# Performance work log

Hardware: AMD Instinct MI355X
Metric: run time of the kernel (lower is better)

## Reference

```python
import jax, jax.numpy as jnp
import numpy as np

B, T, E, H, L, V = 2, 1024, 1024, 16, 4, 32000
HS = E // H
EPS = 1e-5


def layernorm(x, g, b):
    m = jnp.mean(x, axis=-1, keepdims=True)
    v = jnp.mean((x - m) ** 2, axis=-1, keepdims=True)
    return (x - m) * jax.lax.rsqrt(v + EPS) * g + b


def setup_inputs() -> dict:
    key = jax.random.key(0)
    ks = jax.random.split(key, 20)
    s = 0.02
    inp = {
        "ids": jax.random.randint(ks[0], (B, T), 0, V, dtype=jnp.int32),
        "emb": jax.random.normal(ks[1], (V, E), jnp.float32) * s,
        "pos": jax.random.normal(ks[2], (T, E), jnp.float32) * s,
        "wq": jax.random.normal(ks[3], (L, E, E), jnp.float32) * s,
        "bq": jnp.zeros((L, E), jnp.float32),
        "wk": jax.random.normal(ks[4], (L, E, E), jnp.float32) * s,
        "bk": jnp.zeros((L, E), jnp.float32),
        "wv": jax.random.normal(ks[5], (L, E, E), jnp.float32) * s,
        "bv": jnp.zeros((L, E), jnp.float32),
        "w1": jax.random.normal(ks[6], (L, E, 4 * E), jnp.float32) * s,
        "b1": jnp.zeros((L, 4 * E), jnp.float32),
        "w2": jax.random.normal(ks[7], (L, 4 * E, E), jnp.float32) * s,
        "b2": jnp.zeros((L, E), jnp.float32),
        "ln1_g": jnp.ones((L, E), jnp.float32),
        "ln1_b": jnp.zeros((L, E), jnp.float32),
        "ln2_g": jnp.ones((L, E), jnp.float32),
        "ln2_b": jnp.zeros((L, E), jnp.float32),
        "proj_w": jax.random.normal(ks[8], (E, V), jnp.float32) * s,
        "proj_b": jnp.zeros((V,), jnp.float32),
    }
    return inp


def reference(ids, emb, pos, wq, bq, wk, bk, wv, bv, w1, b1, w2, b2,
              ln1_g, ln1_b, ln2_g, ln2_b, proj_w, proj_b):
    x = emb[ids] + pos[:ids.shape[-1]]  # [B,T,E]
    scale = 1.0 / (E ** 0.5)  # NOTE: original divides by embed_size**0.5
    causal = jnp.tril(jnp.ones((T, T), dtype=bool))
    for l in range(L):
        h = layernorm(x, ln1_g[l], ln1_b[l])
        q = (h @ wq[l] + bq[l]).reshape(B, T, H, HS).transpose(0, 2, 1, 3)
        k = (h @ wk[l] + bk[l]).reshape(B, T, H, HS).transpose(0, 2, 1, 3)
        v = (h @ wv[l] + bv[l]).reshape(B, T, H, HS).transpose(0, 2, 1, 3)
        scores = jnp.einsum('bhqd,bhkd->bhqk', q, k) * scale
        scores = jnp.where(causal, scores, -jnp.inf)
        attn = jax.nn.softmax(scores, axis=-1)
        o = jnp.einsum('bhqk,bhkd->bhqd', attn, v)
        o = o.transpose(0, 2, 1, 3).reshape(B, T, E)
        x = x + o
        h2 = layernorm(x, ln2_g[l], ln2_b[l])
        ff = jax.nn.gelu(h2 @ w1[l] + b1[l], approximate=False) @ w2[l] + b2[l]
        x = x + ff  # Dropout(0.2) in eval mode = identity
    logits = x @ proj_w + proj_b  # [B,T,V]
    return logits
```

## Files before the change

### kernel.cpp

```cpp
#include <hip/hip_runtime.h>
#include <hip/hip_bf16.h>
#include <cstdint>

#define B_    2
#define T_    1024
#define E_    1024
#define H_    16
#define HS_   64
#define L_    4
#define V_    32000
#define FF_   4096
#define BT_   2048
#define EPS_  1e-5f
#define SCALE_ 0.03125f

typedef __bf16 bf16;
typedef bf16  bf16x4 __attribute__((ext_vector_type(4)));
typedef bf16  bf16x8 __attribute__((ext_vector_type(8)));
typedef float f32x4  __attribute__((ext_vector_type(4)));

#define GL2LDS(gp, lp) __builtin_amdgcn_global_load_lds( \
    (const __attribute__((address_space(1))) void*)(gp), \
    (__attribute__((address_space(3))) void*)(lp), 16, 0, 0)

__global__ __launch_bounds__(256) void embed_kernel(
    const int* __restrict__ ids, const float* __restrict__ emb,
    const float* __restrict__ pos, float* __restrict__ x)
{
  int bt = blockIdx.x;
  int t  = bt & (T_ - 1);
  int id = ids[bt];
  f32x4 e = *(const f32x4*)(emb + (size_t)id * E_ + threadIdx.x * 4);
  f32x4 p = *(const f32x4*)(pos + (size_t)t  * E_ + threadIdx.x * 4);
  *(f32x4*)(x + (size_t)bt * E_ + threadIdx.x * 4) = e + p;
}

__device__ __forceinline__ float wred_sum(float v) {
#pragma unroll
  for (int o = 32; o; o >>= 1) v += __shfl_xor(v, o, 64);
  return v;
}

__global__ __launch_bounds__(256) void ln_kernel(
    const float* __restrict__ x, const float* __restrict__ g,
    const float* __restrict__ b, bf16* __restrict__ h)
{
  int row = blockIdx.x, tid = threadIdx.x;
  f32x4 v = *(const f32x4*)(x + (size_t)row * E_ + tid * 4);
  float s  = v[0] + v[1] + v[2] + v[3];
  float sq = v[0]*v[0] + v[1]*v[1] + v[2]*v[2] + v[3]*v[3];
  s  = wred_sum(s);
  sq = wred_sum(sq);
  __shared__ float rs[4], rq[4];
  int w = tid >> 6, lane = tid & 63;
  if (lane == 0) { rs[w] = s; rq[w] = sq; }
  __syncthreads();
  float S = rs[0] + rs[1] + rs[2] + rs[3];
  float Q = rq[0] + rq[1] + rq[2] + rq[3];
  float mean = S * (1.0f / E_);
  float var  = Q * (1.0f / E_) - mean * mean;
  float rstd = rsqrtf(fmaxf(var, 0.0f) + EPS_);
  f32x4 gv = *(const f32x4*)(g + tid * 4);
  f32x4 bv = *(const f32x4*)(b + tid * 4);
  f32x4 o = (v - mean) * rstd * gv + bv;
  bf16x4 ob = { (bf16)o[0], (bf16)o[1], (bf16)o[2], (bf16)o[3] };
  *(bf16x4*)(h + (size_t)row * E_ + tid * 4) = ob;
}

__global__ __launch_bounds__(256) void convw_kernel(
    const float* __restrict__ W0, const float* __restrict__ W1, const float* __restrict__ W2,
    bf16* __restrict__ O0, bf16* __restrict__ O1, bf16* __restrict__ O2,
    int K, int ldW)
{
  int z = blockIdx.z;
  const float* W = (z == 0) ? W0 : (z == 1) ? W1 : W2;
  bf16*        O = (z == 0) ? O0 : (z == 1) ? O1 : O2;
  __shared__ float tl[32][33];
  int n0 = blockIdx.x * 32, k0 = blockIdx.y * 32;
  int c = threadIdx.x & 31, r = threadIdx.x >> 5;
#pragma unroll
  for (int p = 0; p < 4; ++p)
    tl[r + p * 8][c] = W[(size_t)(k0 + r + p * 8) * ldW + n0 + c];
  __syncthreads();
#pragma unroll
  for (int p = 0; p < 4; ++p)
    O[(size_t)(n0 + r + p * 8) * K + k0 + c] = (bf16)tl[c][r + p * 8];
}

template <int ACT, int MODE>
__global__ __launch_bounds__(256) void gemm_bf16(
    const bf16* __restrict__ A,
    const bf16* __restrict__ B0, const bf16* __restrict__ B1, const bf16* __restrict__ B2,
    const float* __restrict__ bi0, const float* __restrict__ bi1, const float* __restrict__ bi2,
    bf16* __restrict__ Cb0, bf16* __restrict__ Cb1, bf16* __restrict__ Cb2,
    float* __restrict__ Cf, const float* __restrict__ R,
    int K, int ldc, int LDK)
{
  int z = blockIdx.z;
  const bf16*  Bm = (MODE == 3) ? B0 : (z == 0) ? B0 : (z == 1) ? B1 : B2;
  const float* bi = (z == 0) ? bi0 : (z == 1) ? bi1 : bi2;
  bf16*        Cb = (z == 0) ? Cb0 : (z == 1) ? Cb1 : Cb2;
  int koff = (MODE == 3) ? z * K : 0;

  int nb  = (int)(gridDim.x * gridDim.y);
  int lin = blockIdx.x + gridDim.x * blockIdx.y;
  int per = nb >> 3;
  int b   = (lin & 7) * per + (lin >> 3);
  int mi  = b & 15;
  int ni  = b >> 4;

  __shared__ __align__(16) char lds[2][16384];

  int tid = threadIdx.x;
  int lane = tid & 63, wid = tid >> 6;
  int wm = (wid >> 1) * 64, wn = (wid & 1) * 64;
  int fr = lane & 15, fb = lane >> 4;

  const bf16* Asrc = A  + (size_t)(mi * 128) * LDK + koff;
  const bf16* Bsrc = Bm + (size_t)(ni * 128) * LDK + koff;

  int NT = K >> 5;

#define STAGE(buf, kk)                                                          \
  {                                                                             \
    _Pragma("unroll")                                                           \
    for (int is = 0; is < 2; ++is) {                                            \
      int rl = is * 64 + (tid >> 2);                                            \
      int key = (rl >> 1) & 3;                                                  \
      int ck  = ((tid & 3) ^ key) * 8;                                          \
      GL2LDS(Asrc + (size_t)rl * LDK + (kk) + ck,                               \
             lds[buf] + is * 4096 + tid * 16);                                  \
      GL2LDS(Bsrc + (size_t)rl * LDK + (kk) + ck,                               \
             lds[buf] + 8192 + is * 4096 + tid * 16);                           \
    }                                                                           \
  }

  f32x4 acc[4][4];
#pragma unroll
  for (int i = 0; i < 4; ++i)
#pragma unroll
    for (int j = 0; j < 4; ++j) acc[i][j] = (f32x4){0.f, 0.f, 0.f, 0.f};

  STAGE(0, 0);
  int cur = 0;

  for (int t = 0; t < NT; ++t) {
    __syncthreads();
    if (t + 1 < NT) STAGE(cur ^ 1, (t + 1) << 5);

    const char* Ab = lds[cur];
    const char* Bb = lds[cur] + 8192;
    bf16x8 af[4], bfr[4];
#pragma unroll
    for (int i = 0; i < 4; ++i) {
      int rl = wm + i * 16 + fr;
      af[i] = *(const bf16x8*)(Ab + rl * 64 + ((fb ^ ((rl >> 1) & 3)) * 16));
    }
#pragma unroll
    for (int j = 0; j < 4; ++j) {
      int rl = wn + j * 16 + fr;
      bfr[j] = *(const bf16x8*)(Bb + rl * 64 + ((fb ^ ((rl >> 1) & 3)) * 16));
    }
#pragma unroll
    for (int i = 0; i < 4; ++i)
#pragma unroll
      for (int j = 0; j < 4; ++j)
        acc[i][j] = __builtin_amdgcn_mfma_f32_16x16x32_bf16(af[i], bfr[j], acc[i][j], 0, 0, 0);
    cur ^= 1;
  }
#undef STAGE

#pragma unroll
  for (int i = 0; i < 4; ++i) {
#pragma unroll
    for (int j = 0; j < 4; ++j) {
      int gc = ni * 128 + wn + j * 16 + fr;
      float bv = (MODE == 3) ? 0.f : bi[gc];
#pragma unroll
      for (int r = 0; r < 4; ++r) {
        int gr = mi * 128 + wm + i * 16 + fb * 4 + r;
        float vv = acc[i][j][r] + bv;
        if (ACT == 1) vv = 0.5f * vv * (1.0f + erff(vv * 0.70710678118654752f));
        if (MODE == 2) {
          float nv = vv + R[(size_t)gr * ldc + gc];
          Cf[(size_t)gr * ldc + gc] = nv;
          Cb[(size_t)gr * ldc + gc] = (bf16)nv;
        } else if (MODE == 1) {
          Cb[(size_t)gr * ldc + gc] = (bf16)vv;
        } else if (MODE == 3) {
          Cf[(size_t)(z * BT_ + gr) * ldc + gc] = vv;
        }
      }
    }
  }
}

__global__ __launch_bounds__(256) void combine_kernel(
    const float* __restrict__ p, const float* __restrict__ bi,
    float* __restrict__ x, bf16* __restrict__ xb)
{
  int row = blockIdx.x, tid = threadIdx.x;
  size_t off = (size_t)row * E_ + tid * 4;
  f32x4 a = *(const f32x4*)(p + off);
  f32x4 c = *(const f32x4*)(p + (size_t)BT_ * E_ + off);
  f32x4 bv = *(const f32x4*)(bi + tid * 4);
  f32x4 xv = *(const f32x4*)(x + off);
  f32x4 nv = xv + a + c + bv;
  *(f32x4*)(x + off) = nv;
  bf16x4 ob = { (bf16)nv[0], (bf16)nv[1], (bf16)nv[2], (bf16)nv[3] };
  *(bf16x4*)(xb + off) = ob;
}

__global__ __launch_bounds__(512, 2) void gemm256_kernel(
    const bf16* __restrict__ A, const bf16* __restrict__ Bm,
    const float* __restrict__ bi, float* __restrict__ C, int K, int N)
{
  int nwg = (int)gridDim.x;
  int per = nwg >> 3;
  int bid = (int)blockIdx.x;
  int tl  = (bid & 7) * per + (bid >> 3);
  int mi  = tl & 7, ni = tl >> 3;

  __shared__ __align__(16) char lds[2][65536];

  int tid = threadIdx.x;
  int lane = tid & 63, wid = tid >> 6;
  int wr = wid >> 2, wc = wid & 3;
  int fr = lane & 15, fb = lane >> 4;

  const bf16* Asrc = A  + (size_t)(mi * 256) * K;
  const bf16* Bsrc = Bm + (size_t)(ni * 256) * K;

  int NT = K >> 6;

#define STAGE256(buf, kk)                                                  \
  { _Pragma("unroll")                                                      \
    for (int h = 0; h < 2; ++h) {                                          \
      _Pragma("unroll")                                                    \
      for (int is = 0; is < 2; ++is) {                                     \
        int ri  = is * 64 + (tid >> 3);                                    \
        int ck  = (tid & 7) ^ (ri & 7);                                    \
        int row = h * 128 + ri;                                            \
        GL2LDS(Asrc + (size_t)row * K + (kk) + ck * 8,                     \
               lds[buf] + h * 16384 + is * 8192 + tid * 16);               \
        GL2LDS(Bsrc + (size_t)row * K + (kk) + ck * 8,                     \
               lds[buf] + 32768 + h * 16384 + is * 8192 + tid * 16);       \
      }                                                                    \
    } }

  f32x4 acc[8][4];
#pragma unroll
  for (int i = 0; i < 8; ++i)
#pragma unroll
    for (int j = 0; j < 4; ++j) acc[i][j] = (f32x4){0.f, 0.f, 0.f, 0.f};

  STAGE256(0, 0);

  for (int t = 0; t < NT; ++t) {
    int buf = t & 1;
    if (t + 1 < NT) {
      STAGE256(buf ^ 1, (t + 1) << 6);
      asm volatile("s_waitcnt vmcnt(8)" ::: "memory");
    } else {
      asm volatile("s_waitcnt vmcnt(0)" ::: "memory");
    }
    __builtin_amdgcn_s_barrier();
    asm volatile("" ::: "memory");

    const char* Ab = lds[buf];
    const char* Bb = lds[buf] + 32768;

    bf16x8 bfr[4][2];
#pragma unroll
    for (int n2 = 0; n2 < 4; ++n2) {
      int row = wc * 64 + n2 * 16 + fr;
#pragma unroll
      for (int ks = 0; ks < 2; ++ks)
        bfr[n2][ks] = *(const bf16x8*)(Bb + (row >> 7) * 16384 + (row & 127) * 128
                                          + ((((ks * 4 + fb) ^ (fr & 7))) << 4));
    }
#pragma unroll
    for (int q = 0; q < 4; ++q) {
      bf16x8 af[2][2];
#pragma unroll
      for (int m2 = 0; m2 < 2; ++m2) {
        int ri = (q * 2 + m2) * 16 + fr;
#pragma unroll
        for (int ks = 0; ks < 2; ++ks)
          af[m2][ks] = *(const bf16x8*)(Ab + wr * 16384 + ri * 128
                                           + ((((ks * 4 + fb) ^ (fr & 7))) << 4));
      }
      __builtin_amdgcn_s_setprio(1);
#pragma unroll
      for (int m2 = 0; m2 < 2; ++m2)
#pragma unroll
        for (int n2 = 0; n2 < 4; ++n2)
#pragma unroll
          for (int ks = 0; ks < 2; ++ks)
            acc[q * 2 + m2][n2] = __builtin_amdgcn_mfma_f32_16x16x32_bf16(
                af[m2][ks], bfr[n2][ks], acc[q * 2 + m2][n2], 0, 0, 0);
      __builtin_amdgcn_s_setprio(0);
    }
    asm volatile("" ::: "memory");
    __builtin_amdgcn_s_barrier();
  }
#undef STAGE256

#pragma unroll
  for (int i = 0; i < 8; ++i) {
#pragma unroll
    for (int j = 0; j < 4; ++j) {
      int gc = ni * 256 + wc * 64 + j * 16 + fr;
      float bv = bi[gc];
#pragma unroll
      for (int r = 0; r < 4; ++r) {
        int gr = mi * 256 + wr * 128 + i * 16 + fb * 4 + r;
        C[(size_t)gr * N + gc] = acc[i][j][r] + bv;
      }
    }
  }
}

__global__ __launch_bounds__(256) void attn_kernel(
    const bf16* __restrict__ q, const bf16* __restrict__ k,
    const bf16* __restrict__ v, float* __restrict__ x)
{
  __shared__ __align__(16) char Ks[8192];
  __shared__ __align__(16) char Vs[8192];
  __shared__ __align__(16) char Ps[8192];

  int tid = threadIdx.x, lane = tid & 63, w = tid >> 6;
  int qt = blockIdx.x, bh = blockIdx.y;
  int b = bh >> 4, h = bh & 15;
  size_t hoff = (size_t)b * T_ * E_ + h * HS_;
  int fr = lane & 15, fb = lane >> 4;

  bf16x8 qa[2];
  {
    const bf16* qp = q + hoff + (size_t)(qt * 64 + w * 16 + fr) * E_ + fb * 8;
    qa[0] = *(const bf16x8*)qp;
    qa[1] = *(const bf16x8*)(qp + 32);
  }

  f32x4 O[4];
  float m_[4], l_[4];
#pragma unroll
  for (int i = 0; i < 4; ++i) { O[i] = (f32x4){0.f,0.f,0.f,0.f}; m_[i] = -1e30f; l_[i] = 0.f; }

  for (int kt = 0; kt <= qt; ++kt) {
    __syncthreads();
    {
      const bf16* kbase = k + hoff + (size_t)(kt * 64) * E_;
#pragma unroll
      for (int is = 0; is < 2; ++is) {
        int c = is * 32 + (tid >> 3);
        int key = ((c & 7) ^ (c >> 3)) & 7;
        GL2LDS(kbase + (size_t)c * E_ + (((tid & 7) ^ key) * 8),
               Ks + is * 4096 + tid * 16);
      }
    }
#pragma unroll
    for (int p = 0; p < 2; ++p) {
      int row = tid >> 2;
      int d0 = (tid & 3) * 8 + p * 32;
      bf16x8 vv = *(const bf16x8*)(v + hoff + (size_t)(kt * 64 + row) * E_ + d0);
#pragma unroll
      for (int e = 0; e < 8; ++e) {
        int d = d0 + e;
        int key = ((d & 7) ^ (d >> 3)) & 7;
        *(bf16*)(Vs + d * 128 + ((row * 2) ^ (key << 4))) = vv[e];
      }
    }
    __syncthreads();

    f32x4 s[4];
#pragma unroll
    for (int jc = 0; jc < 4; ++jc) {
      s[jc] = (f32x4){0.f, 0.f, 0.f, 0.f};
#pragma unroll
      for (int kc = 0; kc < 2; ++kc) {
        int c = jc * 16 + fr;
        int key = ((c & 7) ^ (c >> 3)) & 7;
        bf16x8 kf = *(const bf16x8*)(Ks + c * 128 + ((kc * 64 + fb * 16) ^ (key << 4)));
        s[jc] = __builtin_amdgcn_mfma_f32_16x16x32_bf16(qa[kc], kf, s[jc], 0, 0, 0);
      }
    }

    char* pbase = Ps + w * 2048;
#pragma unroll
    for (int r = 0; r < 4; ++r) {
      float s0 = s[0][r] * SCALE_, s1 = s[1][r] * SCALE_;
      float s2 = s[2][r] * SCALE_, s3 = s[3][r] * SCALE_;
      int qrow = qt * 64 + w * 16 + fb * 4 + r;
      if (kt == qt) {
        int kc0 = kt * 64 + fr;
        if (kc0      > qrow) s0 = -1e30f;
        if (kc0 + 16 > qrow) s1 = -1e30f;
        if (kc0 + 32 > qrow) s2 = -1e30f;
        if (kc0 + 48 > qrow) s3 = -1e30f;
      }
      float mx = fmaxf(fmaxf(s0, s1), fmaxf(s2, s3));
      mx = fmaxf(mx, __shfl_xor(mx, 1, 16));
      mx = fmaxf(mx, __shfl_xor(mx, 2, 16));
      mx = fmaxf(mx, __shfl_xor(mx, 4, 16));
      mx = fmaxf(mx, __shfl_xor(mx, 8, 16));
      float mnew = fmaxf(m_[r], mx);
      float p0 = __expf(s0 - mnew), p1 = __expf(s1 - mnew);
      float p2 = __expf(s2 - mnew), p3 = __expf(s3 - mnew);
      float rs = p0 + p1 + p2 + p3;
      rs += __shfl_xor(rs, 1, 16);
      rs += __shfl_xor(rs, 2, 16);
      rs += __shfl_xor(rs, 4, 16);
      rs += __shfl_xor(rs, 8, 16);
      float scl = __expf(m_[r] - mnew);
      l_[r] = l_[r] * scl + rs;
      m_[r] = mnew;
#pragma unroll
      for (int jd = 0; jd < 4; ++jd) O[jd][r] *= scl;
      int key2 = (r << 4) ^ (fb << 5);
      char* pr_ = pbase + (fb * 4 + r) * 128;
      *(bf16*)(pr_ + (( 0 + fr * 2) ^ key2)) = (bf16)p0;
      *(bf16*)(pr_ + ((32 + fr * 2) ^ key2)) = (bf16)p1;
      *(bf16*)(pr_ + ((64 + fr * 2) ^ key2)) = (bf16)p2;
      *(bf16*)(pr_ + ((96 + fr * 2) ^ key2)) = (bf16)p3;
    }

#pragma unroll
    for (int kc = 0; kc < 2; ++kc) {
      int key2 = ((fr & 3) << 4) ^ ((fr >> 2) << 5);
      bf16x8 pa = *(const bf16x8*)(pbase + fr * 128 + ((kc * 64 + fb * 16) ^ key2));
#pragma unroll
      for (int jd = 0; jd < 4; ++jd) {
        int d = jd * 16 + fr;
        int key = ((d & 7) ^ (d >> 3)) & 7;
        bf16x8 vf = *(const bf16x8*)(Vs + d * 128 + ((kc * 64 + fb * 16) ^ (key << 4)));
        O[jd] = __builtin_amdgcn_mfma_f32_16x16x32_bf16(pa, vf, O[jd], 0, 0, 0);
      }
    }
  }

#pragma unroll
  for (int r = 0; r < 4; ++r) {
    float inv = 1.0f / l_[r];
    float* xp = x + hoff + (size_t)(qt * 64 + w * 16 + fb * 4 + r) * E_;
#pragma unroll
    for (int jd = 0; jd < 4; ++jd) {
      int d = jd * 16 + fr;
      xp[d] += O[jd][r] * inv;
    }
  }
}

extern "C" void kernel_launch(void* const* d_in, const int* in_sizes, int n_in,
                              void* d_out, int out_size, void* d_ws, size_t ws_size,
                              hipStream_t stream)
{
  const int*   ids  = (const int*)  d_in[0];
  const float* emb  = (const float*)d_in[1];
  const float* pos  = (const float*)d_in[2];
  const float* wq   = (const float*)d_in[3];
  const float* bq   = (const float*)d_in[4];
  const float* wk   = (const float*)d_in[5];
  const float* bk   = (const float*)d_in[6];
  const float* wv   = (const float*)d_in[7];
  const float* bv   = (const float*)d_in[8];
  const float* w1   = (const float*)d_in[9];
  const float* b1   = (const float*)d_in[10];
  const float* w2   = (const float*)d_in[11];
  const float* b2   = (const float*)d_in[12];
  const float* ln1g = (const float*)d_in[13];
  const float* ln1b = (const float*)d_in[14];
  const float* ln2g = (const float*)d_in[15];
  const float* ln2b = (const float*)d_in[16];
  const float* pw   = (const float*)d_in[17];
  const float* pb   = (const float*)d_in[18];
  float* out = (float*)d_out;

  if (ws_size < (size_t)17 * 1024 * 1024 * 4) return;
  float* ws = (float*)d_ws;
  float* x   = ws;
  bf16*  hb  = (bf16*)(ws + (size_t) 2 * 1024 * 1024);
  bf16*  qb  = (bf16*)(ws + (size_t) 3 * 1024 * 1024);
  bf16*  kb  = (bf16*)(ws + (size_t) 4 * 1024 * 1024);
  bf16*  vb  = (bf16*)(ws + (size_t) 5 * 1024 * 1024);
  bf16*  ffb = (bf16*)(ws + (size_t) 6 * 1024 * 1024);
  float* fp  = ws + (size_t)2 * 1024 * 1024;
  bf16*  lwb = (bf16*)(ws + (size_t)10 * 1024 * 1024);
  bf16*  xb  = (bf16*)(ws + (size_t)16 * 1024 * 1024);
  bf16*  pwb = (bf16*)ws;
  bf16*  wqt = lwb;
  bf16*  wkt = lwb + (size_t)1 * 1024 * 1024;
  bf16*  wvt = lwb + (size_t)2 * 1024 * 1024;
  bf16*  w1t = lwb + (size_t)3 * 1024 * 1024;
  bf16*  w2t = lwb + (size_t)7 * 1024 * 1024;

  embed_kernel<<<BT_, 256, 0, stream>>>(ids, emb, pos, x);

  for (int l = 0; l < L_; ++l) {
    const size_t lEE = (size_t)l * E_ * E_;
    const size_t lEF = (size_t)l * E_ * FF_;

    convw_kernel<<<dim3(E_/32, E_/32, 3), 256, 0, stream>>>(
        wq + lEE, wk + lEE, wv + lEE, wqt, wkt, wvt, E_, E_);
    convw_kernel<<<dim3(FF_/32, E_/32, 1), 256, 0, stream>>>(
        w1 + lEF, nullptr, nullptr, w1t, nullptr, nullptr, E_, FF_);
    convw_kernel<<<dim3(E_/32, FF_/32, 1), 256, 0, stream>>>(
        w2 + lEF, nullptr, nullptr, w2t, nullptr, nullptr, FF_, E_);

    ln_kernel<<<BT_, 256, 0, stream>>>(x, ln1g + l*E_, ln1b + l*E_, hb);

    gemm_bf16<0,1><<<dim3(16, E_/128, 3), 256, 0, stream>>>(
        hb, wqt, wkt, wvt, bq + l*E_, bk + l*E_, bv + l*E_,
        qb, kb, vb, nullptr, nullptr, E_, E_, E_);

    attn_kernel<<<dim3(T_/64, B_*H_), 256, 0, stream>>>(qb, kb, vb, x);

    ln_kernel<<<BT_, 256, 0, stream>>>(x, ln2g + l*E_, ln2b + l*E_, hb);

    gemm_bf16<1,1><<<dim3(16, FF_/128, 1), 256, 0, stream>>>(
        hb, w1t, nullptr, nullptr, b1 + (size_t)l*FF_, nullptr, nullptr,
        ffb, nullptr, nullptr, nullptr, nullptr, E_, FF_, E_);

    gemm_bf16<0,3><<<dim3(16, E_/128, 2), 256, 0, stream>>>(
        ffb, w2t, nullptr, nullptr, nullptr, nullptr, nullptr,
        nullptr, nullptr, nullptr, fp, nullptr, FF_/2, E_, FF_);
    combine_kernel<<<BT_, 256, 0, stream>>>(fp, b2 + l*E_, x, xb);
  }

  convw_kernel<<<dim3(V_/32, E_/32, 1), 256, 0, stream>>>(
      pw, nullptr, nullptr, pwb, nullptr, nullptr, E_, V_);
  gemm256_kernel<<<(V_/256) * 8, 512, 0, stream>>>(
      xb, pwb, pb, out, E_, V_);
}
```

Measured before the change: 860.6 us.

## Fuse per-layer weight conversions into one launch and write interleaved QKV buffer

The three per-layer weight transpose/convert launches are merged into a single convw_all kernel that dispatches by block index. The QKV projection now runs as one GEMM over a concatenated 3072-wide transposed weight (wq/wk/wv are contiguous in workspace) and writes a single interleaved [BT,3072] buffer, with per-column bias selection. The attention kernel reads Q, K and V from that buffer with a 3072 stride. The aim is to cut launch overhead and improve GEMM scheduling, at the cost of strided attention loads and a branchy bias lookup.

```diff
diff --git a/kernel.cpp b/kernel.cpp
--- a/kernel.cpp
+++ b/kernel.cpp
@@ -11,6 +11,7 @@
 #define V_    32000
 #define FF_   4096
 #define BT_   2048
+#define QKV_  3072
 #define EPS_  1e-5f
 #define SCALE_ 0.03125f
 
@@ -68,18 +69,48 @@
 }
 
 __global__ __launch_bounds__(256) void convw_kernel(
-    const float* __restrict__ W0, const float* __restrict__ W1, const float* __restrict__ W2,
-    bf16* __restrict__ O0, bf16* __restrict__ O1, bf16* __restrict__ O2,
-    int K, int ldW)
-{
-  int z = blockIdx.z;
-  const float* W = (z == 0) ? W0 : (z == 1) ? W1 : W2;
-  bf16*        O = (z == 0) ? O0 : (z == 1) ? O1 : O2;
+    const float* __restrict__ W0, bf16* __restrict__ O0, int K, int ldW)
+{
   __shared__ float tl[32][33];
   int n0 = blockIdx.x * 32, k0 = blockIdx.y * 32;
   int c = threadIdx.x & 31, r = threadIdx.x >> 5;
 #pragma unroll
   for (int p = 0; p < 4; ++p)
+    tl[r + p * 8][c] = W0[(size_t)(k0 + r + p * 8) * ldW + n0 + c];
+  __syncthreads();
+#pragma unroll
+  for (int p = 0; p < 4; ++p)
+    O0[(size_t)(n0 + r + p * 8) * K + k0 + c] = (bf16)tl[c][r + p * 8];
+}
+
+__global__ __launch_bounds__(256) void convw_all(
+    const float* __restrict__ wq, const float* __restrict__ wk,
+    const float* __restrict__ wv, const float* __restrict__ w1,
+    const float* __restrict__ w2,
+    bf16* __restrict__ oq, bf16* __restrict__ ok, bf16* __restrict__ ov,
+    bf16* __restrict__ o1, bf16* __restrict__ o2)
+{
+  int bid = blockIdx.x;
+  const float* W; bf16* O; int K, ldW, nx, ny;
+  if (bid < 3072) {
+    int z = bid >> 10, rem = bid & 1023;
+    W = (z == 0) ? wq : (z == 1) ? wk : wv;
+    O = (z == 0) ? oq : (z == 1) ? ok : ov;
+    K = 1024; ldW = 1024; nx = rem & 31; ny = rem >> 5;
+  } else if (bid < 7168) {
+    int idx = bid - 3072;
+    W = w1; O = o1; K = 1024; ldW = 4096;
+    nx = idx & 127; ny = idx >> 7;
+  } else {
+    int idx = bid - 7168;
+    W = w2; O = o2; K = 4096; ldW = 1024;
+    nx = idx & 31; ny = idx >> 5;
+  }
+  __shared__ float tl[32][33];
+  int n0 = nx * 32, k0 = ny * 32;
+  int c = threadIdx.x & 31, r = threadIdx.x >> 5;
+#pragma unroll
+  for (int p = 0; p < 4; ++p)
     tl[r + p * 8][c] = W[(size_t)(k0 + r + p * 8) * ldW + n0 + c];
   __syncthreads();
 #pragma unroll
@@ -87,20 +118,14 @@
     O[(size_t)(n0 + r + p * 8) * K + k0 + c] = (bf16)tl[c][r + p * 8];
 }
 
-template <int ACT, int MODE>
+template <int ACT, int MODE, int B3>
 __global__ __launch_bounds__(256) void gemm_bf16(
-    const bf16* __restrict__ A,
-    const bf16* __restrict__ B0, const bf16* __restrict__ B1, const bf16* __restrict__ B2,
+    const bf16* __restrict__ A, const bf16* __restrict__ Bm,
     const float* __restrict__ bi0, const float* __restrict__ bi1, const float* __restrict__ bi2,
-    bf16* __restrict__ Cb0, bf16* __restrict__ Cb1, bf16* __restrict__ Cb2,
-    float* __restrict__ Cf, const float* __restrict__ R,
+    bf16* __restrict__ Cb, float* __restrict__ Cf,
     int K, int ldc, int LDK)
 {
-  int z = blockIdx.z;
-  const bf16*  Bm = (MODE == 3) ? B0 : (z == 0) ? B0 : (z == 1) ? B1 : B2;
-  const float* bi = (z == 0) ? bi0 : (z == 1) ? bi1 : bi2;
-  bf16*        Cb = (z == 0) ? Cb0 : (z == 1) ? Cb1 : Cb2;
-  int koff = (MODE == 3) ? z * K : 0;
+  int koff = (MODE == 3) ? (int)blockIdx.z * K : 0;
 
   int nb  = (int)(gridDim.x * gridDim.y);
   int lin = blockIdx.x + gridDim.x * blockIdx.y;
@@ -175,20 +200,20 @@
 #pragma unroll
     for (int j = 0; j < 4; ++j) {
       int gc = ni * 128 + wn + j * 16 + fr;
-      float bv = (MODE == 3) ? 0.f : bi[gc];
+      float bv;
+      if (MODE == 3)      bv = 0.f;
+      else if (B3)        bv = (gc < 1024) ? bi0[gc]
+                             : (gc < 2048) ? bi1[gc - 1024] : bi2[gc - 2048];
+      else                bv = bi0[gc];
 #pragma unroll
       for (int r = 0; r < 4; ++r) {
         int gr = mi * 128 + wm + i * 16 + fb * 4 + r;
         float vv = acc[i][j][r] + bv;
         if (ACT == 1) vv = 0.5f * vv * (1.0f + erff(vv * 0.70710678118654752f));
-        if (MODE == 2) {
-          float nv = vv + R[(size_t)gr * ldc + gc];
-          Cf[(size_t)gr * ldc + gc] = nv;
-          Cb[(size_t)gr * ldc + gc] = (bf16)nv;
-        } else if (MODE == 1) {
+        if (MODE == 1) {
           Cb[(size_t)gr * ldc + gc] = (bf16)vv;
-        } else if (MODE == 3) {
-          Cf[(size_t)(z * BT_ + gr) * ldc + gc] = vv;
+        } else {
+          Cf[(size_t)(blockIdx.z * BT_ + gr) * ldc + gc] = vv;
         }
       }
     }
@@ -322,8 +347,7 @@
 }
 
 __global__ __launch_bounds__(256) void attn_kernel(
-    const bf16* __restrict__ q, const bf16* __restrict__ k,
-    const bf16* __restrict__ v, float* __restrict__ x)
+    const bf16* __restrict__ qkv, float* __restrict__ x)
 {
   __shared__ __align__(16) char Ks[8192];
   __shared__ __align__(16) char Vs[8192];
@@ -332,12 +356,16 @@
   int tid = threadIdx.x, lane = tid & 63, w = tid >> 6;
   int qt = blockIdx.x, bh = blockIdx.y;
   int b = bh >> 4, h = bh & 15;
-  size_t hoff = (size_t)b * T_ * E_ + h * HS_;
+  size_t hq = (size_t)b * T_ * QKV_ + h * HS_;
+  const bf16* qp0 = qkv + hq;
+  const bf16* kp0 = qkv + hq + 1024;
+  const bf16* vp0 = qkv + hq + 2048;
+  size_t hx = (size_t)b * T_ * E_ + h * HS_;
   int fr = lane & 15, fb = lane >> 4;
 
   bf16x8 qa[2];
   {
-    const bf16* qp = q + hoff + (size_t)(qt * 64 + w * 16 + fr) * E_ + fb * 8;
+    const bf16* qp = qp0 + (size_t)(qt * 64 + w * 16 + fr) * QKV_ + fb * 8;
     qa[0] = *(const bf16x8*)qp;
     qa[1] = *(const bf16x8*)(qp + 32);
   }
@@ -350,12 +378,12 @@
   for (int kt = 0; kt <= qt; ++kt) {
     __syncthreads();
     {
-      const bf16* kbase = k + hoff + (size_t)(kt * 64) * E_;
+      const bf16* kbase = kp0 + (size_t)(kt * 64) * QKV_;
 #pragma unroll
       for (int is = 0; is < 2; ++is) {
         int c = is * 32 + (tid >> 3);
         int key = ((c & 7) ^ (c >> 3)) & 7;
-        GL2LDS(kbase + (size_t)c * E_ + (((tid & 7) ^ key) * 8),
+        GL2LDS(kbase + (size_t)c * QKV_ + (((tid & 7) ^ key) * 8),
                Ks + is * 4096 + tid * 16);
       }
     }
@@ -363,7 +391,7 @@
     for (int p = 0; p < 2; ++p) {
       int row = tid >> 2;
       int d0 = (tid & 3) * 8 + p * 32;
-      bf16x8 vv = *(const bf16x8*)(v + hoff + (size_t)(kt * 64 + row) * E_ + d0);
+      bf16x8 vv = *(const bf16x8*)(vp0 + (size_t)(kt * 64 + row) * QKV_ + d0);
 #pragma unroll
       for (int e = 0; e < 8; ++e) {
         int d = d0 + e;
@@ -442,7 +470,7 @@
 #pragma unroll
   for (int r = 0; r < 4; ++r) {
     float inv = 1.0f / l_[r];
-    float* xp = x + hoff + (size_t)(qt * 64 + w * 16 + fb * 4 + r) * E_;
+    float* xp = x + hx + (size_t)(qt * 64 + w * 16 + fb * 4 + r) * E_;
 #pragma unroll
     for (int jd = 0; jd < 4; ++jd) {
       int d = jd * 16 + fr;
@@ -478,16 +506,15 @@
 
   if (ws_size < (size_t)17 * 1024 * 1024 * 4) return;
   float* ws = (float*)d_ws;
-  float* x   = ws;
-  bf16*  hb  = (bf16*)(ws + (size_t) 2 * 1024 * 1024);
-  bf16*  qb  = (bf16*)(ws + (size_t) 3 * 1024 * 1024);
-  bf16*  kb  = (bf16*)(ws + (size_t) 4 * 1024 * 1024);
-  bf16*  vb  = (bf16*)(ws + (size_t) 5 * 1024 * 1024);
-  bf16*  ffb = (bf16*)(ws + (size_t) 6 * 1024 * 1024);
-  float* fp  = ws + (size_t)2 * 1024 * 1024;
-  bf16*  lwb = (bf16*)(ws + (size_t)10 * 1024 * 1024);
-  bf16*  xb  = (bf16*)(ws + (size_t)16 * 1024 * 1024);
-  bf16*  pwb = (bf16*)ws;
+  float* x    = ws;
+  bf16*  hb   = (bf16*)(ws + (size_t) 2 * 1024 * 1024);
+  bf16*  qkvb = (bf16*)(ws + (size_t) 3 * 1024 * 1024);
+  bf16*  ffb  = (bf16*)(ws + (size_t) 6 * 1024 * 1024);
+  float* fp   = ws + (size_t)2 * 1024 * 1024;
+  bf16*  lwb  = (bf16*)(ws + (size_t)10 * 1024 * 1024);
+  bf16*  xb   = (bf16*)(ws + (size_t)16 * 1024 * 1024);
+  bf16*  pwb  = (bf16*)ws;
+  bf16*  wqkvt = lwb;
   bf16*  wqt = lwb;
   bf16*  wkt = lwb + (size_t)1 * 1024 * 1024;
   bf16*  wvt = lwb + (size_t)2 * 1024 * 1024;
@@ -500,35 +527,31 @@
     const size_t lEE = (size_t)l * E_ * E_;
     const size_t lEF = (size_t)l * E_ * FF_;
 
-    convw_kernel<<<dim3(E_/32, E_/32, 3), 256, 0, stream>>>(
-        wq + lEE, wk + lEE, wv + lEE, wqt, wkt, wvt, E_, E_);
-    convw_kernel<<<dim3(FF_/32, E_/32, 1), 256, 0, stream>>>(
-        w1 + lEF, nullptr, nullptr, w1t, nullptr, nullptr, E_, FF_);
-    convw_kernel<<<dim3(E_/32, FF_/32, 1), 256, 0, stream>>>(
-        w2 + lEF, nullptr, nullptr, w2t, nullptr, nullptr, FF_, E_);
+    convw_all<<<11264, 256, 0, stream>>>(
+        wq + lEE, wk + lEE, wv + lEE, w1 + lEF, w2 + lEF,
+        wqt, wkt, wvt, w1t, w2t);
 
     ln_kernel<<<BT_, 256, 0, stream>>>(x, ln1g + l*E_, ln1b + l*E_, hb);
 
-    gemm_bf16<0,1><<<dim3(16, E_/128, 3), 256, 0, stream>>>(
-        hb, wqt, wkt, wvt, bq + l*E_, bk + l*E_, bv + l*E_,
-        qb, kb, vb, nullptr, nullptr, E_, E_, E_);
-
-    attn_kernel<<<dim3(T_/64, B_*H_), 256, 0, stream>>>(qb, kb, vb, x);
+    gemm_bf16<0,1,1><<<dim3(16, QKV_/128, 1), 256, 0, stream>>>(
+        hb, wqkvt, bq + l*E_, bk + l*E_, bv + l*E_,
+        qkvb, nullptr, E_, QKV_, E_);
+
+    attn_kernel<<<dim3(T_/64, B_*H_), 256, 0, stream>>>(qkvb, x);
 
     ln_kernel<<<BT_, 256, 0, stream>>>(x, ln2g + l*E_, ln2b + l*E_, hb);
 
-    gemm_bf16<1,1><<<dim3(16, FF_/128, 1), 256, 0, stream>>>(
-        hb, w1t, nullptr, nullptr, b1 + (size_t)l*FF_, nullptr, nullptr,
-        ffb, nullptr, nullptr, nullptr, nullptr, E_, FF_, E_);
-
-    gemm_bf16<0,3><<<dim3(16, E_/128, 2), 256, 0, stream>>>(
-        ffb, w2t, nullptr, nullptr, nullptr, nullptr, nullptr,
-        nullptr, nullptr, nullptr, fp, nullptr, FF_/2, E_, FF_);
+    gemm_bf16<1,1,0><<<dim3(16, FF_/128, 1), 256, 0, stream>>>(
+        hb, w1t, b1 + (size_t)l*FF_, nullptr, nullptr,
+        ffb, nullptr, E_, FF_, E_);
+
+    gemm_bf16<0,3,0><<<dim3(16, E_/128, 2), 256, 0, stream>>>(
+        ffb, w2t, nullptr, nullptr, nullptr,
+        nullptr, fp, FF_/2, E_, FF_);
     combine_kernel<<<BT_, 256, 0, stream>>>(fp, b2 + l*E_, x, xb);
   }
 
-  convw_kernel<<<dim3(V_/32, E_/32, 1), 256, 0, stream>>>(
-      pw, nullptr, nullptr, pwb, nullptr, nullptr, E_, V_);
+  convw_kernel<<<dim3(V_/32, E_/32), 256, 0, stream>>>(pw, pwb, E_, V_);
   gemm256_kernel<<<(V_/256) * 8, 512, 0, stream>>>(
       xb, pwb, pb, out, E_, V_);
 }
```

Result: slower. 923.1 us (+7.3%).

## Deepen vocab projection GEMM pipeline to four K-32 LDS stages

Applied to the files above, without the earlier changes.

The large output projection GEMM now uses four 32 KB LDS buffers holding K=32 slices instead of two 64 KB buffers holding K=64 slices. Three stages are prefetched ahead, with staged vmcnt waits, to hide global-memory latency better, and the LDS swizzle is adapted to 64-byte rows. The unused MODE 2 residual path and its R argument are also removed from the generic GEMM. In exchange there are twice as many barriers per K loop, and each barrier covers less MFMA work.

```diff
diff --git a/kernel.cpp b/kernel.cpp
--- a/kernel.cpp
+++ b/kernel.cpp
@@ -93,7 +93,7 @@
     const bf16* __restrict__ B0, const bf16* __restrict__ B1, const bf16* __restrict__ B2,
     const float* __restrict__ bi0, const float* __restrict__ bi1, const float* __restrict__ bi2,
     bf16* __restrict__ Cb0, bf16* __restrict__ Cb1, bf16* __restrict__ Cb2,
-    float* __restrict__ Cf, const float* __restrict__ R,
+    float* __restrict__ Cf,
     int K, int ldc, int LDK)
 {
   int z = blockIdx.z;
@@ -181,14 +181,10 @@
         int gr = mi * 128 + wm + i * 16 + fb * 4 + r;
         float vv = acc[i][j][r] + bv;
         if (ACT == 1) vv = 0.5f * vv * (1.0f + erff(vv * 0.70710678118654752f));
-        if (MODE == 2) {
-          float nv = vv + R[(size_t)gr * ldc + gc];
-          Cf[(size_t)gr * ldc + gc] = nv;
-          Cb[(size_t)gr * ldc + gc] = (bf16)nv;
-        } else if (MODE == 1) {
+        if (MODE == 1) {
           Cb[(size_t)gr * ldc + gc] = (bf16)vv;
-        } else if (MODE == 3) {
-          Cf[(size_t)(z * BT_ + gr) * ldc + gc] = vv;
+        } else {
+          Cf[(size_t)(blockIdx.z * BT_ + gr) * ldc + gc] = vv;
         }
       }
     }
@@ -221,7 +217,7 @@
   int tl  = (bid & 7) * per + (bid >> 3);
   int mi  = tl & 7, ni = tl >> 3;
 
-  __shared__ __align__(16) char lds[2][65536];
+  __shared__ __align__(16) char lds[4][32768];
 
   int tid = threadIdx.x;
   int lane = tid & 63, wid = tid >> 6;
@@ -231,21 +227,18 @@
   const bf16* Asrc = A  + (size_t)(mi * 256) * K;
   const bf16* Bsrc = Bm + (size_t)(ni * 256) * K;
 
-  int NT = K >> 6;
-
-#define STAGE256(buf, kk)                                                  \
+  int NT = K >> 5;
+
+#define STG(buf, kk)                                                       \
   { _Pragma("unroll")                                                      \
-    for (int h = 0; h < 2; ++h) {                                          \
-      _Pragma("unroll")                                                    \
-      for (int is = 0; is < 2; ++is) {                                     \
-        int ri  = is * 64 + (tid >> 3);                                    \
-        int ck  = (tid & 7) ^ (ri & 7);                                    \
-        int row = h * 128 + ri;                                            \
-        GL2LDS(Asrc + (size_t)row * K + (kk) + ck * 8,                     \
-               lds[buf] + h * 16384 + is * 8192 + tid * 16);               \
-        GL2LDS(Bsrc + (size_t)row * K + (kk) + ck * 8,                     \
-               lds[buf] + 32768 + h * 16384 + is * 8192 + tid * 16);       \
-      }                                                                    \
+    for (int is = 0; is < 2; ++is) {                                       \
+      int c   = is * 512 + tid;                                            \
+      int row = c >> 2;                                                    \
+      int ck  = ((c & 3) ^ ((row >> 1) & 3)) * 8;                          \
+      GL2LDS(Asrc + (size_t)row * K + (kk) + ck,                           \
+             lds[buf] + c * 16);                                           \
+      GL2LDS(Bsrc + (size_t)row * K + (kk) + ck,                           \
+             lds[buf] + 16384 + c * 16);                                   \
     } }
 
   f32x4 acc[8][4];
@@ -254,13 +247,19 @@
 #pragma unroll
     for (int j = 0; j < 4; ++j) acc[i][j] = (f32x4){0.f, 0.f, 0.f, 0.f};
 
-  STAGE256(0, 0);
+  STG(0, 0);
+  STG(1, 32);
+  STG(2, 64);
 
   for (int t = 0; t < NT; ++t) {
-    int buf = t & 1;
-    if (t + 1 < NT) {
-      STAGE256(buf ^ 1, (t + 1) << 6);
+    int buf = t & 3;
+    if (t + 3 < NT) {
+      STG((t + 3) & 3, (t + 3) << 5);
+      asm volatile("s_waitcnt vmcnt(12)" ::: "memory");
+    } else if (t + 2 < NT) {
       asm volatile("s_waitcnt vmcnt(8)" ::: "memory");
+    } else if (t + 1 < NT) {
+      asm volatile("s_waitcnt vmcnt(4)" ::: "memory");
     } else {
       asm volatile("s_waitcnt vmcnt(0)" ::: "memory");
     }
@@ -268,43 +267,50 @@
     asm volatile("" ::: "memory");
 
     const char* Ab = lds[buf];
-    const char* Bb = lds[buf] + 32768;
-
-    bf16x8 bfr[4][2];
+    const char* Bb = lds[buf] + 16384;
+
+    bf16x8 bfr[4];
 #pragma unroll
     for (int n2 = 0; n2 < 4; ++n2) {
       int row = wc * 64 + n2 * 16 + fr;
-#pragma unroll
-      for (int ks = 0; ks < 2; ++ks)
-        bfr[n2][ks] = *(const bf16x8*)(Bb + (row >> 7) * 16384 + (row & 127) * 128
-                                          + ((((ks * 4 + fb) ^ (fr & 7))) << 4));
-    }
-#pragma unroll
-    for (int q = 0; q < 4; ++q) {
-      bf16x8 af[2][2];
-#pragma unroll
-      for (int m2 = 0; m2 < 2; ++m2) {
-        int ri = (q * 2 + m2) * 16 + fr;
-#pragma unroll
-        for (int ks = 0; ks < 2; ++ks)
-          af[m2][ks] = *(const bf16x8*)(Ab + wr * 16384 + ri * 128
-                                           + ((((ks * 4 + fb) ^ (fr & 7))) << 4));
+      bfr[n2] = *(const bf16x8*)(Bb + row * 64 + ((fb ^ ((row >> 1) & 3)) << 4));
+    }
+    {
+      bf16x8 af[4];
+#pragma unroll
+      for (int i = 0; i < 4; ++i) {
+        int row = wr * 128 + i * 16 + fr;
+        af[i] = *(const bf16x8*)(Ab + row * 64 + ((fb ^ ((row >> 1) & 3)) << 4));
       }
       __builtin_amdgcn_s_setprio(1);
 #pragma unroll
-      for (int m2 = 0; m2 < 2; ++m2)
+      for (int i = 0; i < 4; ++i)
 #pragma unroll
         for (int n2 = 0; n2 < 4; ++n2)
-#pragma unroll
-          for (int ks = 0; ks < 2; ++ks)
-            acc[q * 2 + m2][n2] = __builtin_amdgcn_mfma_f32_16x16x32_bf16(
-                af[m2][ks], bfr[n2][ks], acc[q * 2 + m2][n2], 0, 0, 0);
+          acc[i][n2] = __builtin_amdgcn_mfma_f32_16x16x32_bf16(
+              af[i], bfr[n2], acc[i][n2], 0, 0, 0);
+      __builtin_amdgcn_s_setprio(0);
+    }
+    {
+      bf16x8 af[4];
+#pragma unroll
+      for (int i = 0; i < 4; ++i) {
+        int row = wr * 128 + 64 + i * 16 + fr;
+        af[i] = *(const bf16x8*)(Ab + row * 64 + ((fb ^ ((row >> 1) & 3)) << 4));
+      }
+      __builtin_amdgcn_s_setprio(1);
+#pragma unroll
+      for (int i = 0; i < 4; ++i)
+#pragma unroll
+        for (int n2 = 0; n2 < 4; ++n2)
+          acc[4 + i][n2] = __builtin_amdgcn_mfma_f32_16x16x32_bf16(
+              af[i], bfr[n2], acc[4 + i][n2], 0, 0, 0);
       __builtin_amdgcn_s_setprio(0);
     }
     asm volatile("" ::: "memory");
     __builtin_amdgcn_s_barrier();
   }
-#undef STAGE256
+#undef STG
 
 #pragma unroll
   for (int i = 0; i < 8; ++i) {
@@ -511,7 +517,7 @@
 
     gemm_bf16<0,1><<<dim3(16, E_/128, 3), 256, 0, stream>>>(
         hb, wqt, wkt, wvt, bq + l*E_, bk + l*E_, bv + l*E_,
-        qb, kb, vb, nullptr, nullptr, E_, E_, E_);
+        qb, kb, vb, nullptr, E_, E_, E_);
 
     attn_kernel<<<dim3(T_/64, B_*H_), 256, 0, stream>>>(qb, kb, vb, x);
 
@@ -519,11 +525,11 @@
 
     gemm_bf16<1,1><<<dim3(16, FF_/128, 1), 256, 0, stream>>>(
         hb, w1t, nullptr, nullptr, b1 + (size_t)l*FF_, nullptr, nullptr,
-        ffb, nullptr, nullptr, nullptr, nullptr, E_, FF_, E_);
+        ffb, nullptr, nullptr, nullptr, E_, FF_, E_);
 
     gemm_bf16<0,3><<<dim3(16, E_/128, 2), 256, 0, stream>>>(
         ffb, w2t, nullptr, nullptr, nullptr, nullptr, nullptr,
-        nullptr, nullptr, nullptr, fp, nullptr, FF_/2, E_, FF_);
+        nullptr, nullptr, nullptr, fp, FF_/2, E_, FF_);
     combine_kernel<<<BT_, 256, 0, stream>>>(fp, b2 + l*E_, x, xb);
   }
 
```

Result: no change. 872.1 us (+1.3%).
